# Kernel tuning notes

Measured on AMD Instinct MI355X. Metric: run time of the kernel, lower is better.

The kernel has to match this reference:

```python
import jax, jax.numpy as jnp
import numpy as np

B, C, W, H = 16, 512, 32, 32


def spatial_shift1(y):
    # y: [B, W, H, C]; quartile-wise shifts with edge rows/cols left unchanged
    c = y.shape[-1]
    cq = c // 4
    p0 = jnp.concatenate([y[:, :1, :, 0*cq:1*cq], y[:, :-1, :, 0*cq:1*cq]], axis=1)  # w <- w-1
    p1 = jnp.concatenate([y[:, 1:, :, 1*cq:2*cq], y[:, -1:, :, 1*cq:2*cq]], axis=1)  # w <- w+1
    p2 = jnp.concatenate([y[:, :, :1, 2*cq:3*cq], y[:, :, :-1, 2*cq:3*cq]], axis=2)  # h <- h-1
    p3 = jnp.concatenate([y[:, :, 1:, 3*cq:], y[:, :, -1:, 3*cq:]], axis=2)          # h <- h+1
    return jnp.concatenate([p0, p1, p2, p3], axis=-1)


def spatial_shift2(y):
    # same as shift1 with w/h roles swapped
    c = y.shape[-1]
    cq = c // 4
    p0 = jnp.concatenate([y[:, :, :1, 0*cq:1*cq], y[:, :, :-1, 0*cq:1*cq]], axis=2)  # h <- h-1
    p1 = jnp.concatenate([y[:, :, 1:, 1*cq:2*cq], y[:, :, -1:, 1*cq:2*cq]], axis=2)  # h <- h+1
    p2 = jnp.concatenate([y[:, :1, :, 2*cq:3*cq], y[:, :-1, :, 2*cq:3*cq]], axis=1)  # w <- w-1
    p3 = jnp.concatenate([y[:, 1:, :, 3*cq:], y[:, -1:, :, 3*cq:]], axis=1)          # w <- w+1
    return jnp.concatenate([p0, p1, p2, p3], axis=-1)


def setup_inputs() -> dict:
    key = jax.random.key(0)
    ks = jax.random.split(key, 9)
    s = 0.02
    return {
        "x": jax.random.normal(ks[0], (B, C, W, H), dtype=jnp.float32),
        "w1": jax.random.normal(ks[1], (3 * C, C), dtype=jnp.float32) * s,
        "b1": jax.random.normal(ks[2], (3 * C,), dtype=jnp.float32) * s,
        "wa": jax.random.normal(ks[3], (C, C), dtype=jnp.float32) * s,
        "ba": jax.random.normal(ks[4], (C,), dtype=jnp.float32) * s,
        "wb": jax.random.normal(ks[5], (3 * C, C), dtype=jnp.float32) * s,
        "bb": jax.random.normal(ks[6], (3 * C,), dtype=jnp.float32) * s,
        "w2": jax.random.normal(ks[7], (C, C), dtype=jnp.float32) * s,
        "b2": jax.random.normal(ks[8], (C,), dtype=jnp.float32) * s,
    }


def reference(x, w1, b1, wa, ba, wb, bb, w2, b2):
    c = x.shape[1]
    xp = jnp.transpose(x, (0, 2, 3, 1))                     # [B, W, H, C]
    y = jnp.einsum("bwhc,oc->bwho", xp, w1) + b1            # [B, W, H, 3C]
    x1 = spatial_shift1(y[..., :c])
    x2 = spatial_shift2(y[..., c:2 * c])
    x3 = y[..., 2 * c:]
    # SplitAttention: descriptor a = sum over branches and spatial positions
    a = jnp.sum(x1 + x2 + x3, axis=(1, 2))                  # [B, C]
    hat = jax.nn.gelu(a @ wa.T + ba, approximate=False) @ wb.T + bb  # [B, 3C]
    bar = jax.nn.softmax(hat.reshape(-1, 3, c), axis=1)     # softmax over k=3
    g = bar[:, :, None, None, :]                            # [B, 3, 1, 1, C]
    out = g[:, 0] * x1 + g[:, 1] * x2 + g[:, 2] * x3        # [B, W, H, C]
    z = jnp.einsum("bwhc,oc->bwho", out, w2) + b2           # [B, W, H, C]
    return jnp.transpose(z, (0, 3, 1, 2))                   # [B, C, W, H]
```

## Files before the change

kernel.cpp:

```cpp
#include <hip/hip_runtime.h>
#include <stdint.h>

typedef __bf16 bf16x8 __attribute__((ext_vector_type(8)));
typedef float f32x4 __attribute__((ext_vector_type(4)));

#define B_ 16
#define C_ 512
#define S_ 1024
#define N1 1536

__device__ inline unsigned short f2b(float f) {
    unsigned int u = __builtin_bit_cast(unsigned int, f);
    unsigned int lsb = (u >> 16) & 1u;
    u += 0x7fffu + lsb;
    return (unsigned short)(u >> 16);
}
__device__ inline float b2f(unsigned int s) {
    unsigned int u = (s & 0xffffu) << 16;
    return __builtin_bit_cast(float, u);
}

__device__ inline void gl_lds16(const unsigned short* g, unsigned short* l) {
    __builtin_amdgcn_global_load_lds(
        (const __attribute__((address_space(1))) void*)(g),
        (__attribute__((address_space(3))) void*)(l),
        16, 0, 0);
}

__global__ void transpose_convert_x(const float* __restrict__ x, unsigned short* __restrict__ xT,
                                    const float* __restrict__ w1, const float* __restrict__ w2,
                                    unsigned short* __restrict__ w1b, unsigned short* __restrict__ w2b,
                                    float* __restrict__ sums) {
    if (blockIdx.z == 16) {
        int t = (blockIdx.y * 32 + blockIdx.x) * 256 + threadIdx.y * 32 + threadIdx.x;
#pragma unroll
        for (int it = 0; it < 3; it++) {
            int i = t + it * 131072;
            if (i < 196608) {
                float4 v = ((const float4*)w1)[i];
                ((ushort4*)w1b)[i] = make_ushort4(f2b(v.x), f2b(v.y), f2b(v.z), f2b(v.w));
            } else if (i < 262144) {
                int j = i - 196608;
                float4 v = ((const float4*)w2)[j];
                ((ushort4*)w2b)[j] = make_ushort4(f2b(v.x), f2b(v.y), f2b(v.z), f2b(v.w));
            } else if (i < 292864) {
                int j = i - 262144;
                ((float4*)sums)[j] = make_float4(0.f, 0.f, 0.f, 0.f);
            }
        }
        return;
    }
    __shared__ float tile[32][33];
    int b = blockIdx.z;
    int c0 = blockIdx.y * 32;
    int s0 = blockIdx.x * 32;
    int tx = threadIdx.x, ty = threadIdx.y;
    const float* xp = x + ((size_t)b * C_ + c0) * S_ + s0;
#pragma unroll
    for (int i = 0; i < 4; i++)
        tile[ty + i * 8][tx] = xp[(size_t)(ty + i * 8) * S_ + tx];
    __syncthreads();
    unsigned short* op = xT + ((size_t)b * S_ + s0) * C_ + c0;
#pragma unroll
    for (int i = 0; i < 4; i++)
        op[(size_t)(ty + i * 8) * C_ + tx] = f2b(tile[tx][ty + i * 8]);
}

template <bool TRANS_OUT, bool DO_SUMS>
__global__ __launch_bounds__(256) void gemm_bf16(
    const unsigned short* __restrict__ A,
    const unsigned short* __restrict__ Wt,
    const float* __restrict__ bias,
    void* __restrict__ Cout, int N,
    float* __restrict__ Tsum, float* __restrict__ H0, float* __restrict__ H31,
    float* __restrict__ C0, float* __restrict__ C31)
{
    const int K = 512;
    __shared__ __align__(16) unsigned short As[128 * 64];
    __shared__ __align__(16) unsigned short Bs[128 * 64];
    int m0 = blockIdx.x * 128;
    int n0 = blockIdx.y * 128;
    int tid = threadIdx.x;
    int lane = tid & 63, wid = tid >> 6;
    int wm = (wid >> 1) * 64, wn = (wid & 1) * 64;
    int quad = lane >> 4, l16 = lane & 15;
    const unsigned short* Ab = A + (size_t)m0 * K;
    const unsigned short* Bb = Wt + (size_t)n0 * K;

    f32x4 acc[4][4] = {};

    for (int kt = 0; kt < K; kt += 64) {
        __syncthreads();
#pragma unroll
        for (int i = 0; i < 4; i++) {
            int ch = i * 256 + tid;
            int m = ch >> 3;
            int kc = (ch & 7) ^ (m & 7);
            size_t go = (size_t)m * K + kt + kc * 8;
            gl_lds16(Ab + go, &As[ch * 8]);
            gl_lds16(Bb + go, &Bs[ch * 8]);
        }
        __syncthreads();
#pragma unroll
        for (int kh = 0; kh < 2; kh++) {
            bf16x8 af[4], bfr[4];
#pragma unroll
            for (int t = 0; t < 4; t++) {
                int ra = wm + t * 16 + l16;
                int rb = wn + t * 16 + l16;
                int kq = kh * 4 + quad;
                af[t]  = *(const bf16x8*)&As[ra * 64 + ((kq ^ (ra & 7)) * 8)];
                bfr[t] = *(const bf16x8*)&Bs[rb * 64 + ((kq ^ (rb & 7)) * 8)];
            }
#pragma unroll
            for (int mt = 0; mt < 4; mt++)
#pragma unroll
                for (int nt = 0; nt < 4; nt++)
                    acc[mt][nt] = __builtin_amdgcn_mfma_f32_16x16x32_bf16(af[mt], bfr[nt], acc[mt][nt], 0, 0, 0);
        }
    }

#pragma unroll
    for (int mt = 0; mt < 4; mt++) {
#pragma unroll
        for (int nt = 0; nt < 4; nt++) {
            int n = n0 + wn + nt * 16 + l16;
            float bv = bias[n];
            int mbase = m0 + wm + mt * 16 + quad * 4;
            if (!TRANS_OUT) {
                unsigned short* Y = (unsigned short*)Cout;
#pragma unroll
                for (int r = 0; r < 4; r++)
                    Y[(size_t)(mbase + r) * N + n] = f2b(acc[mt][nt][r] + bv);
            } else {
                float* Z = (float*)Cout;
                int b = mbase >> 10;
                int s = mbase & 1023;
                float4 v = make_float4(acc[mt][nt][0] + bv, acc[mt][nt][1] + bv,
                                       acc[mt][nt][2] + bv, acc[mt][nt][3] + bv);
                *(float4*)(&Z[((size_t)(b * 512 + n)) * 1024 + s]) = v;
            }
        }
    }

    if (DO_SUMS) {
        int b = m0 >> 10;
        int wlo = (m0 & 1023) >> 5;
#pragma unroll
        for (int nt = 0; nt < 4; nt++) {
            int n = n0 + wn + nt * 16 + l16;
            float bv = bias[n];
            float tT = 0.f;
#pragma unroll
            for (int mt = 0; mt < 4; mt++)
#pragma unroll
                for (int r = 0; r < 4; r++) tT += acc[mt][nt][r] + bv;
            tT += __shfl_xor(tT, 16);
            tT += __shfl_xor(tT, 32);
            if (quad == 0) {
                atomicAdd(&Tsum[b * 1536 + n], tT);
                float th0 = acc[0][nt][0] + acc[2][nt][0] + 2.f * bv;
                atomicAdd(&H0[b * 1536 + n], th0);
            }
            if (quad == 3) {
                float th31 = acc[1][nt][3] + acc[3][nt][3] + 2.f * bv;
                atomicAdd(&H31[b * 1536 + n], th31);
            }
            if (wlo == 0 && wm == 0) {
                float tc = 0.f;
#pragma unroll
                for (int mt = 0; mt < 2; mt++)
#pragma unroll
                    for (int r = 0; r < 4; r++) tc += acc[mt][nt][r] + bv;
                tc += __shfl_xor(tc, 16);
                tc += __shfl_xor(tc, 32);
                if (quad == 0) atomicAdd(&C0[b * 1536 + n], tc);
            }
            if (wlo == 28 && wm == 64) {
                float tc = 0.f;
#pragma unroll
                for (int mt = 2; mt < 4; mt++)
#pragma unroll
                    for (int r = 0; r < 4; r++) tc += acc[mt][nt][r] + bv;
                tc += __shfl_xor(tc, 16);
                tc += __shfl_xor(tc, 32);
                if (quad == 0) atomicAdd(&C31[b * 1536 + n], tc);
            }
        }
    }
}

__global__ __launch_bounds__(256) void mlp_layer1(
    const float* __restrict__ sums, const float* __restrict__ wa,
    const float* __restrict__ ba, float* __restrict__ h)
{
    __shared__ float sa[512];
    int b = blockIdx.x >> 7;
    int t = threadIdx.x;
    const float* Tp   = sums;
    const float* H0p  = sums + 24576;
    const float* H31p = sums + 49152;
    const float* C0p  = sums + 73728;
    const float* C31p = sums + 98304;
#pragma unroll
    for (int j = 0; j < 2; j++) {
        int c = t + j * 256;
        int q = c >> 7;
        int n1 = b * 1536 + c;
        float t123 = Tp[n1] + Tp[n1 + 512] + Tp[n1 + 1024];
        float sC1 = C0p[n1] - C31p[n1];
        float sH1 = H0p[n1] - H31p[n1];
        float sC2 = C0p[n1 + 512] - C31p[n1 + 512];
        float sH2 = H0p[n1 + 512] - H31p[n1 + 512];
        float e = (q < 2) ? (sC1 + sH2) : (sH1 + sC2);
        sa[c] = t123 + ((q & 1) ? -e : e);
    }
    __syncthreads();
    int lane = t & 63, wid = t >> 6;
    int o = (blockIdx.x & 127) * 4 + wid;
    const float4* wr = (const float4*)(wa + (size_t)o * 512);
    float4 w0 = wr[lane * 2], w1v = wr[lane * 2 + 1];
    float4 a0 = ((const float4*)sa)[lane * 2], a1 = ((const float4*)sa)[lane * 2 + 1];
    float dot = w0.x * a0.x + w0.y * a0.y + w0.z * a0.z + w0.w * a0.w
              + w1v.x * a1.x + w1v.y * a1.y + w1v.z * a1.z + w1v.w * a1.w;
#pragma unroll
    for (int off = 32; off; off >>= 1) dot += __shfl_down(dot, off);
    if (lane == 0) {
        float v = dot + ba[o];
        h[b * 512 + o] = 0.5f * v * (1.0f + erff(v * 0.7071067811865475f));
    }
}

__global__ __launch_bounds__(256) void mlp_layer2(
    const float* __restrict__ h, const float* __restrict__ wb,
    const float* __restrict__ bb, float* __restrict__ hat)
{
    int gw = (blockIdx.x * 256 + threadIdx.x) >> 6;
    int lane = threadIdx.x & 63;
    int b = gw / 1536;
    int o = gw - b * 1536;
    const float4* wr = (const float4*)(wb + (size_t)o * 512);
    const float4* hr = (const float4*)(h + (size_t)b * 512);
    float4 w0 = wr[lane * 2], w1 = wr[lane * 2 + 1];
    float4 h0 = hr[lane * 2], h1 = hr[lane * 2 + 1];
    float dot = w0.x * h0.x + w0.y * h0.y + w0.z * h0.z + w0.w * h0.w
              + w1.x * h1.x + w1.y * h1.y + w1.z * h1.z + w1.w * h1.w;
#pragma unroll
    for (int off = 32; off; off >>= 1) dot += __shfl_down(dot, off);
    if (lane == 0)
        hat[(size_t)b * 1536 + o] = dot + bb[o];
}

__global__ __launch_bounds__(256) void combine_softmax(
    const unsigned short* __restrict__ y, const float* __restrict__ hat,
    unsigned short* __restrict__ outT)
{
    int b = blockIdx.y;
    int w = blockIdx.x;
    int t = threadIdx.x;
    int h0 = (t >> 6) * 8;
    int c8 = (t & 63) * 8;
    int q = c8 >> 7;
    int dw1 = (q == 0) ? -1 : (q == 1) ? 1 : 0;
    int dh1 = (q == 2) ? -1 : (q == 3) ? 1 : 0;
    int dh2 = (q == 0) ? -1 : (q == 1) ? 1 : 0;
    int dw2 = (q == 2) ? -1 : (q == 3) ? 1 : 0;
    float g0[8], g1[8], g2[8];
#pragma unroll
    for (int j = 0; j < 8; j++) {
        int c = c8 + j;
        float h0v = hat[b * 1536 + c];
        float h1v = hat[b * 1536 + 512 + c];
        float h2v = hat[b * 1536 + 1024 + c];
        float mx = fmaxf(h0v, fmaxf(h1v, h2v));
        float e0 = __expf(h0v - mx), e1 = __expf(h1v - mx), e2 = __expf(h2v - mx);
        float inv = 1.0f / (e0 + e1 + e2);
        g0[j] = e0 * inv; g1[j] = e1 * inv; g2[j] = e2 * inv;
    }
    int w1i = min(max(w + dw1, 0), 31);
    int w2i = min(max(w + dw2, 0), 31);
    size_t base = (size_t)b * S_;
#pragma unroll
    for (int hh = 0; hh < 8; hh++) {
        int h = h0 + hh;
        int h1i = min(max(h + dh1, 0), 31);
        int h2i = min(max(h + dh2, 0), 31);
        uint4 u1 = *(const uint4*)&y[(base + w1i * 32 + h1i) * N1 + c8];
        uint4 u2 = *(const uint4*)&y[(base + w2i * 32 + h2i) * N1 + 512 + c8];
        uint4 u3 = *(const uint4*)&y[(base + w * 32 + h) * N1 + 1024 + c8];
        unsigned int p[4];
        const unsigned int* a1 = &u1.x;
        const unsigned int* a2 = &u2.x;
        const unsigned int* a3 = &u3.x;
#pragma unroll
        for (int k = 0; k < 4; k++) {
            int j = k * 2;
            float lo = g0[j] * b2f(a1[k]) + g1[j] * b2f(a2[k]) + g2[j] * b2f(a3[k]);
            float hi = g0[j + 1] * b2f(a1[k] >> 16) + g1[j + 1] * b2f(a2[k] >> 16) + g2[j + 1] * b2f(a3[k] >> 16);
            p[k] = (unsigned int)f2b(lo) | ((unsigned int)f2b(hi) << 16);
        }
        *(uint4*)&outT[(base + w * 32 + h) * 512 + c8] = make_uint4(p[0], p[1], p[2], p[3]);
    }
}

extern "C" void kernel_launch(void* const* d_in, const int* in_sizes, int n_in,
                              void* d_out, int out_size, void* d_ws, size_t ws_size,
                              hipStream_t stream) {
    const float* x  = (const float*)d_in[0];
    const float* w1 = (const float*)d_in[1];
    const float* b1 = (const float*)d_in[2];
    const float* wa = (const float*)d_in[3];
    const float* ba = (const float*)d_in[4];
    const float* wb = (const float*)d_in[5];
    const float* bb = (const float*)d_in[6];
    const float* w2 = (const float*)d_in[7];
    const float* b2 = (const float*)d_in[8];
    float* out = (float*)d_out;

    char* ws = (char*)d_ws;
    unsigned short* xT   = (unsigned short*)(ws);
    unsigned short* outT = (unsigned short*)(ws);
    unsigned short* w1b  = (unsigned short*)(ws + 16777216);
    unsigned short* w2b  = (unsigned short*)(ws + 18350080);
    unsigned short* y    = (unsigned short*)(ws + 18874368);
    float* sums          = (float*)(ws + 69206016);
    float* h_buf         = (float*)(ws + 69697536);
    float* hat_buf       = (float*)(ws + 69730304);

    float* Tsum = sums;
    float* H0   = sums + 24576;
    float* H31  = sums + 49152;
    float* C0   = sums + 73728;
    float* C31  = sums + 98304;

    transpose_convert_x<<<dim3(32, 16, 17), dim3(32, 8), 0, stream>>>(
        x, xT, w1, w2, w1b, w2b, sums);
    gemm_bf16<false, true><<<dim3(128, 12), dim3(256), 0, stream>>>(
        xT, w1b, b1, (void*)y, 1536, Tsum, H0, H31, C0, C31);
    mlp_layer1<<<dim3(2048), dim3(256), 0, stream>>>(sums, wa, ba, h_buf);
    mlp_layer2<<<dim3(6144), dim3(256), 0, stream>>>(h_buf, wb, bb, hat_buf);
    combine_softmax<<<dim3(32, 16), dim3(256), 0, stream>>>(y, hat_buf, outT);
    gemm_bf16<true, false><<<dim3(128, 4), dim3(256), 0, stream>>>(
        outT, w2b, b2, (void*)out, 512, nullptr, nullptr, nullptr, nullptr, nullptr);
}
```

Before: 180.3 us.

## Replace first GEMM with 256x256-tile, 8-wave, double-buffered pipelined kernel

The first projection GEMM moves to a new kernel with 256x256 block tiles, 512 threads and a two-stage LDS double buffer. Its prefetch of the next K-slice, issued via global_load_lds, is interleaved with MFMA sub-groups using explicit waitcnt, barriers and setprio. The aim is to hide global load latency and raise MFMA utilisation and data reuse compared with the 128x128 single-buffer kernel. In exchange it uses 128KB of LDS per block, issues only 384 blocks, and must remap the fused spatial-sum atomics (H0/H31/C0/C31) to the new tile geometry.

Result: no change. 178.0 us (-1.3%).

```diff
diff --git a/kernel.cpp b/kernel.cpp
--- a/kernel.cpp
+++ b/kernel.cpp
@@ -66,14 +66,161 @@
         op[(size_t)(ty + i * 8) * C_ + tx] = f2b(tile[tx][ty + i * 8]);
 }
 
-template <bool TRANS_OUT, bool DO_SUMS>
+__global__ __launch_bounds__(512, 2) void gemm1_8ph(
+    const unsigned short* __restrict__ A,
+    const unsigned short* __restrict__ Wt,
+    const float* __restrict__ bias,
+    unsigned short* __restrict__ Y,
+    float* __restrict__ Tsum, float* __restrict__ H0, float* __restrict__ H31,
+    float* __restrict__ C0, float* __restrict__ C31)
+{
+    __shared__ __align__(16) unsigned short lds[8 * 8192];
+    const int tid = threadIdx.x;
+    const int lane = tid & 63, wid = tid >> 6;
+    const int wm = (wid >> 2) * 128;
+    const int wn = (wid & 3) * 64;
+    const int quad = lane >> 4, l16 = lane & 15;
+    const int m0 = blockIdx.x * 256;
+    const int n0 = blockIdx.y * 256;
+    const int ahalf = wid >> 2;
+    const int bhalf = (wid & 3) >> 1;
+    const int rb0 = (wid & 1) * 64;
+    const unsigned short* Ab = A + (size_t)m0 * 512;
+    const unsigned short* Bb = Wt + (size_t)n0 * 512;
+
+    f32x4 acc[8][4] = {};
+
+    auto stage = [&](int T, int part) {
+        const unsigned short* src = (part < 2) ? (Ab + (size_t)part * 128 * 512)
+                                               : (Bb + (size_t)(part - 2) * 128 * 512);
+        unsigned short* dst = &lds[(size_t)((T & 1) * 4 + part) * 8192];
+#pragma unroll
+        for (int i = 0; i < 2; i++) {
+            int ch = i * 512 + tid;
+            int r = ch >> 3, kc = ch & 7;
+            size_t go = (size_t)r * 512 + T * 64 + ((kc ^ (r & 7)) * 8);
+            gl_lds16(src + go, dst + ch * 8);
+        }
+    };
+
+    stage(0, 2); stage(0, 3); stage(0, 0); stage(0, 1);
+    stage(1, 2); stage(1, 3);
+    asm volatile("s_waitcnt vmcnt(4)" ::: "memory");
+    __builtin_amdgcn_s_barrier();
+
+    bf16x8 bfr[4][2];
+    for (int T = 0; T < 8; T++) {
+        const unsigned short* Asl = &lds[(size_t)((T & 1) * 4 + ahalf) * 8192];
+        const unsigned short* Bsl = &lds[(size_t)((T & 1) * 4 + 2 + bhalf) * 8192];
+#pragma unroll
+        for (int sg = 0; sg < 4; sg++) {
+            bf16x8 af[2][2];
+            if (sg == 0) {
+#pragma unroll
+                for (int n = 0; n < 4; n++)
+#pragma unroll
+                    for (int kh = 0; kh < 2; kh++) {
+                        int rb = rb0 + n * 16 + l16;
+                        bfr[n][kh] = *(const bf16x8*)&Bsl[rb * 64 + (((kh * 4 + quad) ^ (rb & 7)) * 8)];
+                    }
+            }
+#pragma unroll
+            for (int mi = 0; mi < 2; mi++)
+#pragma unroll
+                for (int kh = 0; kh < 2; kh++) {
+                    int ra = (sg * 2 + mi) * 16 + l16;
+                    af[mi][kh] = *(const bf16x8*)&Asl[ra * 64 + (((kh * 4 + quad) ^ (ra & 7)) * 8)];
+                }
+            if (sg == 0) { if (T < 7) stage(T + 1, 0); }
+            else if (sg == 1) { if (T < 7) stage(T + 1, 1); }
+            else if (sg == 2) { if (T < 6) stage(T + 2, 2); }
+            else {
+                if (T < 6) stage(T + 2, 3);
+                if (T < 6)       asm volatile("s_waitcnt vmcnt(4)" ::: "memory");
+                else if (T == 6) asm volatile("s_waitcnt vmcnt(0)" ::: "memory");
+            }
+            __builtin_amdgcn_s_barrier();
+            asm volatile("s_waitcnt lgkmcnt(0)" ::: "memory");
+            __builtin_amdgcn_sched_barrier(0);
+            __builtin_amdgcn_s_setprio(1);
+#pragma unroll
+            for (int mi = 0; mi < 2; mi++)
+#pragma unroll
+                for (int n = 0; n < 4; n++)
+#pragma unroll
+                    for (int kh = 0; kh < 2; kh++)
+                        acc[sg * 2 + mi][n] = __builtin_amdgcn_mfma_f32_16x16x32_bf16(
+                            af[mi][kh], bfr[n][kh], acc[sg * 2 + mi][n], 0, 0, 0);
+            __builtin_amdgcn_s_setprio(0);
+            __builtin_amdgcn_s_barrier();
+        }
+    }
+
+#pragma unroll
+    for (int m = 0; m < 8; m++)
+#pragma unroll
+        for (int nt = 0; nt < 4; nt++) {
+            int n = n0 + wn + nt * 16 + l16;
+            float bv = bias[n];
+            int mbase = m0 + wm + m * 16 + quad * 4;
+#pragma unroll
+            for (int r = 0; r < 4; r++)
+                Y[(size_t)(mbase + r) * N1 + n] = f2b(acc[m][nt][r] + bv);
+        }
+
+    {
+        int b = m0 >> 10;
+        int wlo = (m0 & 1023) >> 5;
+#pragma unroll
+        for (int nt = 0; nt < 4; nt++) {
+            int n = n0 + wn + nt * 16 + l16;
+            float bv = bias[n];
+            float tT = 0.f;
+#pragma unroll
+            for (int m = 0; m < 8; m++)
+#pragma unroll
+                for (int r = 0; r < 4; r++) tT += acc[m][nt][r] + bv;
+            tT += __shfl_xor(tT, 16);
+            tT += __shfl_xor(tT, 32);
+            if (quad == 0) {
+                atomicAdd(&Tsum[b * 1536 + n], tT);
+                float th0 = acc[0][nt][0] + acc[2][nt][0] + acc[4][nt][0] + acc[6][nt][0] + 4.f * bv;
+                atomicAdd(&H0[b * 1536 + n], th0);
+            }
+            if (quad == 3) {
+                float th31 = acc[1][nt][3] + acc[3][nt][3] + acc[5][nt][3] + acc[7][nt][3] + 4.f * bv;
+                atomicAdd(&H31[b * 1536 + n], th31);
+            }
+            if (wlo == 0 && wm == 0) {
+                float tc = 0.f;
+#pragma unroll
+                for (int m = 0; m < 2; m++)
+#pragma unroll
+                    for (int r = 0; r < 4; r++) tc += acc[m][nt][r] + bv;
+                tc += __shfl_xor(tc, 16);
+                tc += __shfl_xor(tc, 32);
+                if (quad == 0) atomicAdd(&C0[b * 1536 + n], tc);
+            }
+            if (wlo == 24 && wm == 128) {
+                float tc = 0.f;
+#pragma unroll
+                for (int m = 6; m < 8; m++)
+#pragma unroll
+                    for (int r = 0; r < 4; r++) tc += acc[m][nt][r] + bv;
+                tc += __shfl_xor(tc, 16);
+                tc += __shfl_xor(tc, 32);
+                if (quad == 0) atomicAdd(&C31[b * 1536 + n], tc);
+            }
+        }
+    }
+}
+
+template <bool TRANS_OUT>
 __global__ __launch_bounds__(256) void gemm_bf16(
     const unsigned short* __restrict__ A,
     const unsigned short* __restrict__ Wt,
     const float* __restrict__ bias,
-    void* __restrict__ Cout, int N,
-    float* __restrict__ Tsum, float* __restrict__ H0, float* __restrict__ H31,
-    float* __restrict__ C0, float* __restrict__ C31)
+    void* __restrict__ Cout, int N)
 {
     const int K = 512;
     __shared__ __align__(16) unsigned short As[128 * 64];
@@ -128,10 +275,10 @@
             float bv = bias[n];
             int mbase = m0 + wm + mt * 16 + quad * 4;
             if (!TRANS_OUT) {
-                unsigned short* Y = (unsigned short*)Cout;
+                unsigned short* Yp = (unsigned short*)Cout;
 #pragma unroll
                 for (int r = 0; r < 4; r++)
-                    Y[(size_t)(mbase + r) * N + n] = f2b(acc[mt][nt][r] + bv);
+                    Yp[(size_t)(mbase + r) * N + n] = f2b(acc[mt][nt][r] + bv);
             } else {
                 float* Z = (float*)Cout;
                 int b = mbase >> 10;
@@ -139,52 +286,6 @@
                 float4 v = make_float4(acc[mt][nt][0] + bv, acc[mt][nt][1] + bv,
                                        acc[mt][nt][2] + bv, acc[mt][nt][3] + bv);
                 *(float4*)(&Z[((size_t)(b * 512 + n)) * 1024 + s]) = v;
-            }
-        }
-    }
-
-    if (DO_SUMS) {
-        int b = m0 >> 10;
-        int wlo = (m0 & 1023) >> 5;
-#pragma unroll
-        for (int nt = 0; nt < 4; nt++) {
-            int n = n0 + wn + nt * 16 + l16;
-            float bv = bias[n];
-            float tT = 0.f;
-#pragma unroll
-            for (int mt = 0; mt < 4; mt++)
-#pragma unroll
-                for (int r = 0; r < 4; r++) tT += acc[mt][nt][r] + bv;
-            tT += __shfl_xor(tT, 16);
-            tT += __shfl_xor(tT, 32);
-            if (quad == 0) {
-                atomicAdd(&Tsum[b * 1536 + n], tT);
-                float th0 = acc[0][nt][0] + acc[2][nt][0] + 2.f * bv;
-                atomicAdd(&H0[b * 1536 + n], th0);
-            }
-            if (quad == 3) {
-                float th31 = acc[1][nt][3] + acc[3][nt][3] + 2.f * bv;
-                atomicAdd(&H31[b * 1536 + n], th31);
-            }
-            if (wlo == 0 && wm == 0) {
-                float tc = 0.f;
-#pragma unroll
-                for (int mt = 0; mt < 2; mt++)
-#pragma unroll
-                    for (int r = 0; r < 4; r++) tc += acc[mt][nt][r] + bv;
-                tc += __shfl_xor(tc, 16);
-                tc += __shfl_xor(tc, 32);
-                if (quad == 0) atomicAdd(&C0[b * 1536 + n], tc);
-            }
-            if (wlo == 28 && wm == 64) {
-                float tc = 0.f;
-#pragma unroll
-                for (int mt = 2; mt < 4; mt++)
-#pragma unroll
-                    for (int r = 0; r < 4; r++) tc += acc[mt][nt][r] + bv;
-                tc += __shfl_xor(tc, 16);
-                tc += __shfl_xor(tc, 32);
-                if (quad == 0) atomicAdd(&C31[b * 1536 + n], tc);
             }
         }
     }
@@ -335,11 +436,11 @@
 
     transpose_convert_x<<<dim3(32, 16, 17), dim3(32, 8), 0, stream>>>(
         x, xT, w1, w2, w1b, w2b, sums);
-    gemm_bf16<false, true><<<dim3(128, 12), dim3(256), 0, stream>>>(
-        xT, w1b, b1, (void*)y, 1536, Tsum, H0, H31, C0, C31);
+    gemm1_8ph<<<dim3(64, 6), dim3(512), 0, stream>>>(
+        xT, w1b, b1, y, Tsum, H0, H31, C0, C31);
     mlp_layer1<<<dim3(2048), dim3(256), 0, stream>>>(sums, wa, ba, h_buf);
     mlp_layer2<<<dim3(6144), dim3(256), 0, stream>>>(h_buf, wb, bb, hat_buf);
     combine_softmax<<<dim3(32, 16), dim3(256), 0, stream>>>(y, hat_buf, outT);
-    gemm_bf16<true, false><<<dim3(128, 4), dim3(256), 0, stream>>>(
-        outT, w2b, b2, (void*)out, 512, nullptr, nullptr, nullptr, nullptr, nullptr);
-}
+    gemm_bf16<true><<<dim3(128, 4), dim3(256), 0, stream>>>(
+        outT, w2b, b2, (void*)out, 512);
+}
```

## Rewrite GEMMs as double-buffered 128x256 tiles with LDS-staged coalesced epilogues

Applied to the files above, without the earlier changes.

Replaces the single-buffered 128x128 GEMM with a 512-thread, 128x256 tile kernel. It double-buffers A and B in LDS, prefetches the next K-slices while MFMAs run in two phases with explicit waitcnt, barriers and setprio, and stages output through swizzled LDS so global stores are 16-byte coalesced, including the transposed fp32 output. The aim is to hide global load latency and cut uncoalesced epilogue stores. In exchange it needs 96KB of LDS per block, which may limit occupancy, and the hand-placed waitcnts add correctness risk. The DO_SUMS tail is not shown and may still assume the old tile width.

Result: no change. 177.3 us (-1.7%).

```diff
diff --git a/kernel.cpp b/kernel.cpp
--- a/kernel.cpp
+++ b/kernel.cpp
@@ -67,79 +67,165 @@
 }
 
 template <bool TRANS_OUT, bool DO_SUMS>
-__global__ __launch_bounds__(256) void gemm_bf16(
+__global__ __launch_bounds__(512, 2) void gemm_2ph(
     const unsigned short* __restrict__ A,
     const unsigned short* __restrict__ Wt,
     const float* __restrict__ bias,
-    void* __restrict__ Cout, int N,
+    void* __restrict__ Cout,
     float* __restrict__ Tsum, float* __restrict__ H0, float* __restrict__ H31,
     float* __restrict__ C0, float* __restrict__ C31)
 {
-    const int K = 512;
-    __shared__ __align__(16) unsigned short As[128 * 64];
-    __shared__ __align__(16) unsigned short Bs[128 * 64];
-    int m0 = blockIdx.x * 128;
-    int n0 = blockIdx.y * 128;
-    int tid = threadIdx.x;
-    int lane = tid & 63, wid = tid >> 6;
-    int wm = (wid >> 1) * 64, wn = (wid & 1) * 64;
-    int quad = lane >> 4, l16 = lane & 15;
-    const unsigned short* Ab = A + (size_t)m0 * K;
-    const unsigned short* Bb = Wt + (size_t)n0 * K;
+    __shared__ __align__(16) unsigned short lds[49152];
+    const int tid = threadIdx.x;
+    const int lane = tid & 63, wid = tid >> 6;
+    const int wm = (wid >> 2) * 64;
+    const int wn = (wid & 3) * 64;
+    const int quad = lane >> 4, l16 = lane & 15;
+    const int m0 = blockIdx.x * 128;
+    const int n0 = blockIdx.y * 256;
+    const unsigned short* Ab = A + (size_t)m0 * 512;
+    const unsigned short* Bb = Wt + (size_t)n0 * 512;
 
     f32x4 acc[4][4] = {};
 
-    for (int kt = 0; kt < K; kt += 64) {
+    auto stageA = [&](int T) {
+        unsigned short* dst = &lds[(T & 1) * 8192];
+#pragma unroll
+        for (int i = 0; i < 2; i++) {
+            int ch = i * 512 + tid;
+            int r = ch >> 3, kc = ch & 7;
+            gl_lds16(Ab + (size_t)r * 512 + T * 64 + ((kc ^ (r & 7)) * 8), dst + ch * 8);
+        }
+    };
+    auto stageB = [&](int T) {
+        unsigned short* dst = &lds[16384 + (T & 1) * 16384];
+#pragma unroll
+        for (int i = 0; i < 4; i++) {
+            int ch = i * 512 + tid;
+            int r = ch >> 3, kc = ch & 7;
+            gl_lds16(Bb + (size_t)r * 512 + T * 64 + ((kc ^ (r & 7)) * 8), dst + ch * 8);
+        }
+    };
+
+    stageB(0); stageA(0); stageB(1);
+    asm volatile("s_waitcnt vmcnt(4)" ::: "memory");
+    __builtin_amdgcn_s_barrier();
+
+    for (int T = 0; T < 8; T++) {
+        const unsigned short* Asl = &lds[(T & 1) * 8192];
+        const unsigned short* Bsl = &lds[16384 + (T & 1) * 16384];
+        bf16x8 bfr[4][2], af[2][2];
+#pragma unroll
+        for (int nt = 0; nt < 4; nt++)
+#pragma unroll
+            for (int kh = 0; kh < 2; kh++) {
+                int rb = wn + nt * 16 + l16;
+                bfr[nt][kh] = *(const bf16x8*)&Bsl[rb * 64 + (((kh * 4 + quad) ^ (rb & 7)) * 8)];
+            }
+#pragma unroll
+        for (int mi = 0; mi < 2; mi++)
+#pragma unroll
+            for (int kh = 0; kh < 2; kh++) {
+                int ra = wm + mi * 16 + l16;
+                af[mi][kh] = *(const bf16x8*)&Asl[ra * 64 + (((kh * 4 + quad) ^ (ra & 7)) * 8)];
+            }
+        if (T < 7) stageA(T + 1);
+        __builtin_amdgcn_s_barrier();
+        asm volatile("s_waitcnt lgkmcnt(0)" ::: "memory");
+        __builtin_amdgcn_sched_barrier(0);
+        __builtin_amdgcn_s_setprio(1);
+#pragma unroll
+        for (int mi = 0; mi < 2; mi++)
+#pragma unroll
+            for (int nt = 0; nt < 4; nt++)
+#pragma unroll
+                for (int kh = 0; kh < 2; kh++)
+                    acc[mi][nt] = __builtin_amdgcn_mfma_f32_16x16x32_bf16(
+                        af[mi][kh], bfr[nt][kh], acc[mi][nt], 0, 0, 0);
+        __builtin_amdgcn_s_setprio(0);
+        __builtin_amdgcn_s_barrier();
+#pragma unroll
+        for (int mi = 0; mi < 2; mi++)
+#pragma unroll
+            for (int kh = 0; kh < 2; kh++) {
+                int ra = wm + (2 + mi) * 16 + l16;
+                af[mi][kh] = *(const bf16x8*)&Asl[ra * 64 + (((kh * 4 + quad) ^ (ra & 7)) * 8)];
+            }
+        if (T < 6) {
+            stageB(T + 2);
+            asm volatile("s_waitcnt vmcnt(4)" ::: "memory");
+        } else if (T == 6) {
+            asm volatile("s_waitcnt vmcnt(0)" ::: "memory");
+        }
+        __builtin_amdgcn_s_barrier();
+        asm volatile("s_waitcnt lgkmcnt(0)" ::: "memory");
+        __builtin_amdgcn_sched_barrier(0);
+        __builtin_amdgcn_s_setprio(1);
+#pragma unroll
+        for (int mi = 0; mi < 2; mi++)
+#pragma unroll
+            for (int nt = 0; nt < 4; nt++)
+#pragma unroll
+                for (int kh = 0; kh < 2; kh++)
+                    acc[2 + mi][nt] = __builtin_amdgcn_mfma_f32_16x16x32_bf16(
+                        af[mi][kh], bfr[nt][kh], acc[2 + mi][nt], 0, 0, 0);
+        __builtin_amdgcn_s_setprio(0);
+        __builtin_amdgcn_s_barrier();
+    }
+
+    if (!TRANS_OUT) {
+        unsigned short* eb = lds;
+#pragma unroll
+        for (int mt = 0; mt < 4; mt++)
+#pragma unroll
+            for (int nt = 0; nt < 4; nt++) {
+                int col = wn + nt * 16 + l16;
+                float bv = bias[n0 + col];
+                int cc = col >> 3, cw = col & 7;
+#pragma unroll
+                for (int r = 0; r < 4; r++) {
+                    int row = wm + mt * 16 + quad * 4 + r;
+                    eb[row * 256 + (((cc ^ (row & 7)) << 3) + cw)] = f2b(acc[mt][nt][r] + bv);
+                }
+            }
         __syncthreads();
-#pragma unroll
-        for (int i = 0; i < 4; i++) {
-            int ch = i * 256 + tid;
-            int m = ch >> 3;
-            int kc = (ch & 7) ^ (m & 7);
-            size_t go = (size_t)m * K + kt + kc * 8;
-            gl_lds16(Ab + go, &As[ch * 8]);
-            gl_lds16(Bb + go, &Bs[ch * 8]);
-        }
-        __syncthreads();
-#pragma unroll
-        for (int kh = 0; kh < 2; kh++) {
-            bf16x8 af[4], bfr[4];
-#pragma unroll
-            for (int t = 0; t < 4; t++) {
-                int ra = wm + t * 16 + l16;
-                int rb = wn + t * 16 + l16;
-                int kq = kh * 4 + quad;
-                af[t]  = *(const bf16x8*)&As[ra * 64 + ((kq ^ (ra & 7)) * 8)];
-                bfr[t] = *(const bf16x8*)&Bs[rb * 64 + ((kq ^ (rb & 7)) * 8)];
-            }
-#pragma unroll
-            for (int mt = 0; mt < 4; mt++)
-#pragma unroll
-                for (int nt = 0; nt < 4; nt++)
-                    acc[mt][nt] = __builtin_amdgcn_mfma_f32_16x16x32_bf16(af[mt], bfr[nt], acc[mt][nt], 0, 0, 0);
-        }
-    }
-
-#pragma unroll
-    for (int mt = 0; mt < 4; mt++) {
-#pragma unroll
-        for (int nt = 0; nt < 4; nt++) {
-            int n = n0 + wn + nt * 16 + l16;
-            float bv = bias[n];
-            int mbase = m0 + wm + mt * 16 + quad * 4;
-            if (!TRANS_OUT) {
-                unsigned short* Y = (unsigned short*)Cout;
-#pragma unroll
-                for (int r = 0; r < 4; r++)
-                    Y[(size_t)(mbase + r) * N + n] = f2b(acc[mt][nt][r] + bv);
-            } else {
-                float* Z = (float*)Cout;
-                int b = mbase >> 10;
-                int s = mbase & 1023;
-                float4 v = make_float4(acc[mt][nt][0] + bv, acc[mt][nt][1] + bv,
-                                       acc[mt][nt][2] + bv, acc[mt][nt][3] + bv);
-                *(float4*)(&Z[((size_t)(b * 512 + n)) * 1024 + s]) = v;
-            }
+        unsigned short* Y = (unsigned short*)Cout;
+#pragma unroll
+        for (int it = 0; it < 8; it++) {
+            int cid = it * 512 + tid;
+            int row = cid >> 5, j = cid & 31;
+            bf16x8 v = *(const bf16x8*)&eb[row * 256 + ((j ^ (row & 7)) << 3)];
+            *(bf16x8*)&Y[(size_t)(m0 + row) * N1 + n0 + j * 8] = v;
+        }
+    } else {
+        float* ef = (float*)lds;
+        int b = m0 >> 10, s0r = m0 & 1023;
+        float* O = (float*)Cout;
+#pragma unroll
+        for (int p = 0; p < 2; p++) {
+            if (((wid & 3) >> 1) == p) {
+#pragma unroll
+                for (int mt = 0; mt < 4; mt++)
+#pragma unroll
+                    for (int nt = 0; nt < 4; nt++) {
+                        int nl = wn - p * 128 + nt * 16 + l16;
+                        float bv = bias[n0 + p * 128 + nl];
+                        int c = (wm >> 2) + mt * 4 + quad;
+                        f32x4 v;
+#pragma unroll
+                        for (int r = 0; r < 4; r++) v[r] = acc[mt][nt][r] + bv;
+                        *(f32x4*)&ef[nl * 128 + ((c ^ (nl & 7)) << 2)] = v;
+                    }
+            }
+            __syncthreads();
+#pragma unroll
+            for (int it = 0; it < 8; it++) {
+                int cid = it * 512 + tid;
+                int nl = cid >> 5, j = cid & 31;
+                f32x4 v = *(const f32x4*)&ef[nl * 128 + ((j ^ (nl & 7)) << 2)];
+                *(f32x4*)&O[((size_t)(b * 512 + n0 + p * 128 + nl)) * 1024 + s0r + j * 4] = v;
+            }
+            if (p == 0) __syncthreads();
         }
     }
 
@@ -335,11 +421,11 @@
 
     transpose_convert_x<<<dim3(32, 16, 17), dim3(32, 8), 0, stream>>>(
         x, xT, w1, w2, w1b, w2b, sums);
-    gemm_bf16<false, true><<<dim3(128, 12), dim3(256), 0, stream>>>(
-        xT, w1b, b1, (void*)y, 1536, Tsum, H0, H31, C0, C31);
+    gemm_2ph<false, true><<<dim3(128, 6), dim3(512), 0, stream>>>(
+        xT, w1b, b1, (void*)y, Tsum, H0, H31, C0, C31);
     mlp_layer1<<<dim3(2048), dim3(256), 0, stream>>>(sums, wa, ba, h_buf);
     mlp_layer2<<<dim3(6144), dim3(256), 0, stream>>>(h_buf, wb, bb, hat_buf);
     combine_softmax<<<dim3(32, 16), dim3(256), 0, stream>>>(y, hat_buf, outT);
-    gemm_bf16<true, false><<<dim3(128, 4), dim3(256), 0, stream>>>(
-        outT, w2b, b2, (void*)out, 512, nullptr, nullptr, nullptr, nullptr, nullptr);
-}
+    gemm_2ph<true, false><<<dim3(128, 2), dim3(512), 0, stream>>>(
+        outT, w2b, b2, (void*)out, nullptr, nullptr, nullptr, nullptr, nullptr);
+}
```
